# Performance work log

Hardware: AMD Instinct MI355X
Metric: run time of the kernel (lower is better)

Reference implementation:

```python
import jax, jax.numpy as jnp
import numpy as np

D_MODEL = 1024
NUM_HEADS = 16
D_HEAD = 64
D_MLP = 4096
SEQ = 2048
BATCH = 4
NEG_BIG = 1e10


def setup_inputs() -> dict:
    key = jax.random.key(0)
    ks = jax.random.split(key, 10)
    s = 1.0 / np.sqrt(D_MODEL)
    return {
        "x": jax.random.normal(ks[0], (BATCH, SEQ, D_MODEL), dtype=jnp.float32),
        "W_K": jax.random.normal(ks[1], (NUM_HEADS, D_HEAD, D_MODEL), dtype=jnp.float32) * s,
        "W_Q": jax.random.normal(ks[2], (NUM_HEADS, D_HEAD, D_MODEL), dtype=jnp.float32) * s,
        "W_V": jax.random.normal(ks[3], (NUM_HEADS, D_HEAD, D_MODEL), dtype=jnp.float32) * s,
        "W_O": jax.random.normal(ks[4], (D_MODEL, D_HEAD * NUM_HEADS), dtype=jnp.float32) * s,
        "W_in": jax.random.normal(ks[5], (D_MLP, D_MODEL), dtype=jnp.float32) * s,
        "b_in": jnp.zeros((D_MLP,), dtype=jnp.float32),
        "W_out": jax.random.normal(ks[6], (D_MODEL, D_MLP), dtype=jnp.float32) * s,
        "b_out": jnp.zeros((D_MODEL,), dtype=jnp.float32),
    }


def _block(x, W_K, W_Q, W_V, W_O, W_in, b_in, W_out, b_out):
    seq = x.shape[1]
    # Attention
    k = jnp.einsum("ihd,bpd->biph", W_K, x)
    q = jnp.einsum("ihd,bpd->biph", W_Q, x)
    v = jnp.einsum("ihd,bpd->biph", W_V, x)
    scores = jnp.einsum("biph,biqh->biqp", k, q)  # [b, i, q(query), p(key)]
    mask = jnp.tril(jnp.ones((seq, seq), dtype=x.dtype))  # causal: key p <= query q
    scores = scores * mask - NEG_BIG * (1.0 - mask)
    attn = jax.nn.softmax(scores / np.sqrt(D_HEAD), axis=-1)
    z = jnp.einsum("biph,biqp->biqh", v, attn)  # [b, heads, q, d_head]
    z_flat = jnp.transpose(z, (0, 2, 1, 3)).reshape(z.shape[0], seq, -1)  # b q (i h)
    attn_out = jnp.einsum("df,bqf->bqd", W_O, z_flat)
    x = x + attn_out
    # MLP
    h = jnp.einsum("md,bpd->bpm", W_in, x) + b_in
    h = jax.nn.gelu(h, approximate=False)
    mlp_out = jnp.einsum("dm,bpm->bpd", W_out, h) + b_out
    return x + mlp_out


def reference(x, W_K, W_Q, W_V, W_O, W_in, b_in, W_out, b_out):
    return _block(x, W_K, W_Q, W_V, W_O, W_in, b_in, W_out, b_out)
```

## Files before the change

### kernel.cpp

```cpp
#include <hip/hip_runtime.h>
#include <hip/hip_bf16.h>

typedef __bf16 bf16;
typedef __bf16 bf16x8 __attribute__((ext_vector_type(8)));
typedef __bf16 bf16x4 __attribute__((ext_vector_type(4)));
typedef float  f32x4  __attribute__((ext_vector_type(4)));

#define MFMA(a,b,c) __builtin_amdgcn_mfma_f32_16x16x32_bf16(a,b,c,0,0,0)
#define EXP2F(x) __builtin_amdgcn_exp2f(x)

__device__ __forceinline__ void gload16(const void* g, void* l) {
  __builtin_amdgcn_global_load_lds((__attribute__((address_space(1))) void*)(g),
                                   (__attribute__((address_space(3))) void*)(l), 16, 0, 0);
}

__global__ void cast_kernel(const float* __restrict__ in, bf16* __restrict__ out, int n8) {
  int i = blockIdx.x * 256 + threadIdx.x;
  if (i >= n8) return;
  const float4* p = (const float4*)in;
  float4 a = p[2*i], b = p[2*i+1];
  bf16x8 v;
  v[0]=(bf16)a.x; v[1]=(bf16)a.y; v[2]=(bf16)a.z; v[3]=(bf16)a.w;
  v[4]=(bf16)b.x; v[5]=(bf16)b.y; v[6]=(bf16)b.z; v[7]=(bf16)b.w;
  *(bf16x8*)(out + (size_t)8*i) = v;
}

__device__ __forceinline__ float gelu_t(float s) {
  float u = s * (0.7978845608f + 0.0356774081f * s * s);
  return s / (1.0f + EXP2F(-2.885390082f * u));
}

#define LGKM0_FENCE() { asm volatile("s_waitcnt lgkmcnt(0)" ::: "memory"); \
                        __builtin_amdgcn_sched_barrier(0); }

#define LDA_PH(MI2) { _Pragma("unroll") for (int i = 0; i < 4; i++) { \
    af[i][0] = *(const bf16x8*)(lds + ab + ((((MI2)<<2)+i) << 11) + rdswz); \
    af[i][1] = *(const bf16x8*)(lds + ab + ((((MI2)<<2)+i) << 11) + 1024 + rdswz); } }

#define LDB_PH(NI2) { _Pragma("unroll") for (int n = 0; n < 2; n++) { \
    bfr[((NI2)<<1)+n][0] = *(const bf16x8*)(lds + bb + (((((NI2)<<1)+n)) << 11) + rdswz); \
    bfr[((NI2)<<1)+n][1] = *(const bf16x8*)(lds + bb + (((((NI2)<<1)+n)) << 11) + 1024 + rdswz); } }

#define MM_PH(MI2, NI2) { __builtin_amdgcn_s_setprio(1); \
    _Pragma("unroll") for (int i = 0; i < 4; i++) \
      _Pragma("unroll") for (int n = 0; n < 2; n++) { \
        acc[((MI2)<<2)+i][((NI2)<<1)+n] = MFMA(af[i][0], bfr[((NI2)<<1)+n][0], acc[((MI2)<<2)+i][((NI2)<<1)+n]); \
        acc[((MI2)<<2)+i][((NI2)<<1)+n] = MFMA(af[i][1], bfr[((NI2)<<1)+n][1], acc[((MI2)<<2)+i][((NI2)<<1)+n]); } \
    __builtin_amdgcn_s_setprio(0); }

#define GTILE(CUR, S1, S2, VM) { \
    const int ab = ((CUR) << 16) + (wm << 14); \
    const int bb = ((CUR) << 16) + 32768 + (wn << 13); \
    LDA_PH(0); LDB_PH(0); \
    if (S1) STG(sA, (CUR)^1, 0, 1, t + 1); \
    asm volatile("s_waitcnt lgkmcnt(8)" ::: "memory"); \
    __builtin_amdgcn_s_barrier(); LGKM0_FENCE(); \
    MM_PH(0, 0); \
    LDB_PH(1); \
    if (S2) STG(sB, (CUR), 1, 0, t + 2); \
    __builtin_amdgcn_s_barrier(); LGKM0_FENCE(); \
    MM_PH(0, 1); \
    LDA_PH(1); \
    if (S2) STG(sB, (CUR), 1, 1, t + 2); \
    __builtin_amdgcn_s_barrier(); LGKM0_FENCE(); \
    MM_PH(1, 0); \
    if (S2) STG(sA, (CUR), 0, 0, t + 2); \
    MM_PH(1, 1); \
    asm volatile("s_waitcnt vmcnt(" #VM ")" ::: "memory"); \
    __builtin_amdgcn_s_barrier(); \
    __builtin_amdgcn_sched_barrier(0); }

template<int EPI>
__global__ __launch_bounds__(512, 2) void gemm256(
    const bf16* __restrict__ A, const bf16* __restrict__ B,
    float* __restrict__ outf, bf16* __restrict__ outb,
    const float* __restrict__ add, const float* __restrict__ bias,
    bf16* __restrict__ vtb,
    int M, int N, int K, int gx)
{
  __shared__ __attribute__((aligned(128))) char lds[131072];
  const int tid = threadIdx.x;
  const int w = tid >> 6, l = tid & 63, lg = l >> 4, li = l & 15;
  const int wm = w >> 2, wn = w & 3;

  const int nwg = gridDim.x, orig = blockIdx.x;
  const int q = nwg >> 3, r = nwg & 7;
  const int xcd = orig & 7, pos = orig >> 3;
  const int wg = (xcd < r ? xcd*(q+1) : r*(q+1) + (xcd-r)*q) + pos;
  const int m0 = (wg / gx) << 8, n0 = (wg % gx) << 8;

  const int NT = K >> 6;

  const int srow = ((tid >> 7) << 4) + ((tid >> 2) & 15);
  const int scol = (((tid >> 6) & 1) << 5) + (((tid & 3) << 3) ^ (((tid >> 5) & 1) << 4));
  const bf16* sA = A + (size_t)(m0 + srow) * K + scol;
  const bf16* sB = B + (size_t)(n0 + srow) * K + scol;
  char* const myl = lds + (w << 10);

  auto STG = [&](const bf16* s0, int buf, int isB, int h, int tt) {
    const bf16* g = s0 + ((size_t)(h << 7)) * K + ((size_t)tt << 6);
    char* lb = myl + (buf << 16) + (isB << 15) + (h << 14);
    gload16(g, lb);
    gload16(g + ((size_t)K << 6), lb + 8192);
  };

  const int rdswz = (li << 6) + ((lg << 4) ^ ((li & 8) << 2));

  f32x4 acc[8][4] = {};
  bf16x8 af[4][2], bfr[4][2];

  STG(sB, 0, 1, 0, 0); STG(sB, 0, 1, 1, 0); STG(sA, 0, 0, 0, 0); STG(sA, 0, 0, 1, 0);
  asm volatile("s_waitcnt vmcnt(4)" ::: "memory");
  STG(sB, 1, 1, 0, 1); STG(sB, 1, 1, 1, 1); STG(sA, 1, 0, 0, 1);
  asm volatile("s_waitcnt vmcnt(6)" ::: "memory");
  __builtin_amdgcn_s_barrier();
  __builtin_amdgcn_sched_barrier(0);

  int t = 0;
  for (int tt = 0; tt + 3 < NT; tt += 2) {
    t = tt;     GTILE(0, 1, 1, 6);
    t = tt + 1; GTILE(1, 1, 1, 6);
  }
  t = NT - 2; GTILE(0, 1, 0, 0);
  t = NT - 1; GTILE(1, 0, 0, 0);

  if (EPI == 0 && n0 >= 2048) {
    #pragma unroll
    for (int mi = 0; mi < 8; mi++) {
      const int row = m0 + (wm << 7) + (mi << 4) + (lg << 2);
      const int p = row & 2047;
      const size_t bhb = (size_t)((row >> 11) << 4);
      #pragma unroll
      for (int ni = 0; ni < 4; ni++) {
        const int col = n0 + (wn << 6) + (ni << 4) + li;
        const int hh = (col >> 6) & 15, dd = col & 63;
        bf16x4 pk;
        pk[0] = (bf16)acc[mi][ni][0]; pk[1] = (bf16)acc[mi][ni][1];
        pk[2] = (bf16)acc[mi][ni][2]; pk[3] = (bf16)acc[mi][ni][3];
        *(bf16x4*)(vtb + ((bhb + hh) * 64 + dd) * 2048 + p) = pk;
      }
    }
    return;
  }

  #pragma unroll
  for (int mi = 0; mi < 8; mi++) {
    const int row = m0 + (wm << 7) + (mi << 4) + (lg << 2);
    #pragma unroll
    for (int ni = 0; ni < 4; ni++) {
      const int col = n0 + (wn << 6) + (ni << 4) + li;
      #pragma unroll
      for (int r2 = 0; r2 < 4; r2++) {
        const size_t idx = (size_t)(row + r2) * N + col;
        float v = acc[mi][ni][r2];
        if (EPI == 0) {
          outb[idx] = (bf16)v;
        } else if (EPI == 1) {
          float s = v + add[idx];
          outf[idx] = s; outb[idx] = (bf16)s;
        } else if (EPI == 2) {
          outb[idx] = (bf16)gelu_t(v + bias[col]);
        } else {
          outf[idx] = v + bias[col] + add[idx];
        }
      }
    }
  }
}

#define N_LDA2(BMI) { _Pragma("unroll") for (int i = 0; i < 2; i++) { \
    af[i][0] = *(const bf16x8*)(lds + abase + (((BMI)+i) << 11) + rdswz); \
    af[i][1] = *(const bf16x8*)(lds + abase + (((BMI)+i) << 11) + 1024 + rdswz); } }

#define N_LDB2(BNI) { _Pragma("unroll") for (int n = 0; n < 2; n++) { \
    bfr[(BNI)+n][0] = *(const bf16x8*)(lds + bbase + (((BNI)+n) << 11) + rdswz); \
    bfr[(BNI)+n][1] = *(const bf16x8*)(lds + bbase + (((BNI)+n) << 11) + 1024 + rdswz); } }

#define N_MMQ(MB, NB) { __builtin_amdgcn_s_setprio(1); \
    _Pragma("unroll") for (int i = 0; i < 2; i++) \
      _Pragma("unroll") for (int n = 0; n < 2; n++) { \
        acc[((MB)<<1)+i][((NB)<<1)+n] = MFMA(af[i][0], bfr[((NB)<<1)+n][0], acc[((MB)<<1)+i][((NB)<<1)+n]); \
        acc[((MB)<<1)+i][((NB)<<1)+n] = MFMA(af[i][1], bfr[((NB)<<1)+n][1], acc[((MB)<<1)+i][((NB)<<1)+n]); } \
    __builtin_amdgcn_s_setprio(0); }

#define NTILE(CUR, S1, S2, VM) { \
    const int abase = (CUR) * 49152 + ((wm >> 1) << 14) + ((wm & 1) << 13); \
    const int bbase = (CUR) * 49152 + 32768 + (wn << 13); \
    N_LDA2(0); N_LDB2(0); \
    if (S1) STA((CUR)^1, 1, t + 1); \
    __builtin_amdgcn_s_barrier(); LGKM0_FENCE(); \
    N_MMQ(0, 0); \
    N_LDB2(2); \
    if (S2) STB((CUR), 0, t + 2); \
    __builtin_amdgcn_s_barrier(); LGKM0_FENCE(); \
    N_MMQ(0, 1); \
    N_LDA2(2); \
    if (S2) STB((CUR), 1, t + 2); \
    __builtin_amdgcn_s_barrier(); LGKM0_FENCE(); \
    N_MMQ(1, 0); \
    if (S2) STA((CUR), 0, t + 2); \
    N_MMQ(1, 1); \
    asm volatile("s_waitcnt vmcnt(" #VM ")" ::: "memory"); \
    __builtin_amdgcn_s_barrier(); \
    __builtin_amdgcn_sched_barrier(0); }

template<int EPI>
__global__ __launch_bounds__(512, 2) void gemm128n(
    const bf16* __restrict__ A, const bf16* __restrict__ B,
    float* __restrict__ outf, bf16* __restrict__ outb,
    const float* __restrict__ add, const float* __restrict__ bias,
    int M, int N, int K, int gx)
{
  __shared__ __attribute__((aligned(128))) char lds[98304];
  const int tid = threadIdx.x;
  const int w = tid >> 6, l = tid & 63, lg = l >> 4, li = l & 15;
  const int wm = w >> 1, wn = w & 1;

  const int nwg = gridDim.x, orig = blockIdx.x;
  const int q = nwg >> 3, r = nwg & 7;
  const int xcd = orig & 7, pos = orig >> 3;
  const int wg = (xcd < r ? xcd*(q+1) : r*(q+1) + (xcd-r)*q) + pos;
  const int m0 = (wg / gx) << 8, n0 = (wg % gx) << 7;

  const int NT = K >> 6;

  const int srow = ((tid >> 7) << 4) + ((tid >> 2) & 15);
  const int scol = (((tid >> 6) & 1) << 5) + (((tid & 3) << 3) ^ (((tid >> 5) & 1) << 4));
  const bf16* sA = A + (size_t)(m0 + srow) * K + scol;
  const bf16* sB = B + (size_t)(n0 + srow) * K + scol;
  char* const myl = lds + (w << 10);

  auto STA = [&](int buf, int h, int tt) {
    const bf16* g = sA + ((size_t)(h << 7)) * K + ((size_t)tt << 6);
    char* lb = myl + buf * 49152 + (h << 14);
    gload16(g, lb);
    gload16(g + ((size_t)K << 6), lb + 8192);
  };
  auto STB = [&](int buf, int h, int tt) {
    const bf16* g = sB + ((size_t)(h << 6)) * K + ((size_t)tt << 6);
    gload16(g, myl + buf * 49152 + 32768 + (h << 13));
  };

  const int rdswz = (li << 6) + ((lg << 4) ^ ((li & 8) << 2));

  f32x4 acc[4][4] = {};
  bf16x8 af[2][2], bfr[4][2];

  STB(0, 0, 0); STB(0, 1, 0); STA(0, 0, 0); STA(0, 1, 0);
  STB(1, 0, 1); STB(1, 1, 1); STA(1, 0, 1);
  asm volatile("s_waitcnt vmcnt(4)" ::: "memory");
  __builtin_amdgcn_s_barrier();
  __builtin_amdgcn_sched_barrier(0);

  int t = 0;
  for (int tt = 0; tt + 3 < NT; tt += 2) {
    t = tt;     NTILE(0, 1, 1, 4);
    t = tt + 1; NTILE(1, 1, 1, 4);
  }
  t = NT - 2; NTILE(0, 1, 0, 0);
  t = NT - 1; NTILE(1, 0, 0, 0);

  #pragma unroll
  for (int mi = 0; mi < 4; mi++) {
    const int row = m0 + (wm << 6) + (mi << 4) + (lg << 2);
    #pragma unroll
    for (int ni = 0; ni < 4; ni++) {
      const int col = n0 + (wn << 6) + (ni << 4) + li;
      #pragma unroll
      for (int r2 = 0; r2 < 4; r2++) {
        const size_t idx = (size_t)(row + r2) * N + col;
        float v = acc[mi][ni][r2];
        if (EPI == 0) {
          outb[idx] = (bf16)v;
        } else if (EPI == 1) {
          float s = v + add[idx];
          outf[idx] = s; outb[idx] = (bf16)s;
        } else if (EPI == 2) {
          outb[idx] = (bf16)gelu_t(v + bias[col]);
        } else {
          outf[idx] = v + bias[col] + add[idx];
        }
      }
    }
  }
}

__global__ __launch_bounds__(256) void attn_kernel(const bf16* __restrict__ qkv,
                                                   const bf16* __restrict__ vt,
                                                   bf16* __restrict__ z)
{
  __shared__ bf16 Ksh[2][64*64];
  __shared__ bf16 Vsh[2][64*64];
  __shared__ bf16 Pl[4*16*64];

  const int tid = threadIdx.x;
  const int w = tid >> 6, l = tid & 63, lg = l >> 4, li = l & 15;
  const int pr = blockIdx.x & 15, bh = blockIdx.x >> 4;
  const int h = bh & 15, b = bh >> 4;
  const size_t tb = (size_t)b * 2048;

  const int srow = tid >> 3, sc = tid & 7;
  const bf16* Kg = qkv + (tb + srow) * 3072 + 1024 + (h << 6) + ((sc ^ (srow & 7)) << 3);
  const bf16* Vg = vt + ((size_t)bh * 64 + srow) * 2048 + ((sc ^ (srow & 7)) << 3);

  char* pw = (char*)Pl + (w << 11) + li * 128;
  const int psw = (li & 3) << 5;

  for (int hf = 0; hf < 2; ++hf) {
    const int qt = hf ? pr : (31 - pr);
    const int qw = (qt << 6) + (w << 4);

    const bf16* Qp = qkv + (tb + qw + li) * 3072 + (h << 6);
    bf16x8 qa0 = *(const bf16x8*)(Qp + (lg << 3));
    bf16x8 qa1 = *(const bf16x8*)(Qp + 32 + (lg << 3));
    #pragma unroll
    for (int e = 0; e < 8; e++) {
      qa0[e] = (bf16)((float)qa0[e] * 0.1803368801f);
      qa1[e] = (bf16)((float)qa1[e] * 0.1803368801f);
    }

    f32x4 zacc[4] = {};
    float mR = -1e30f, lS = 0.f;
    const int nkt = qt + 1;

    gload16(Kg,                   (bf16*)Ksh[0] + (w << 9));
    gload16(Kg + (size_t)32*3072, (bf16*)Ksh[0] + 2048 + (w << 9));
    gload16(Vg,                   (bf16*)Vsh[0] + (w << 9));
    gload16(Vg + (size_t)32*2048, (bf16*)Vsh[0] + 2048 + (w << 9));
    __syncthreads();

    for (int kt = 0; kt < nkt; ++kt) {
      const int cur = kt & 1;
      const int pb = kt << 6;

      if (kt + 1 < nkt) {
        const int nb = cur ^ 1;
        const size_t ko = (size_t)(pb + 64) * 3072;
        gload16(Kg + ko,                   (bf16*)Ksh[nb] + (w << 9));
        gload16(Kg + ko + (size_t)32*3072, (bf16*)Ksh[nb] + 2048 + (w << 9));
        gload16(Vg + pb + 64,                   (bf16*)Vsh[nb] + (w << 9));
        gload16(Vg + pb + 64 + (size_t)32*2048, (bf16*)Vsh[nb] + 2048 + (w << 9));
      }

      f32x4 s[4];
      __builtin_amdgcn_s_setprio(1);
      #pragma unroll
      for (int sub = 0; sub < 4; ++sub) {
        const char* kr = (const char*)Ksh[cur] + ((sub << 4) + li) * 128;
        const int c0 = (lg ^ (li & 7)) << 4;
        bf16x8 kb0 = *(const bf16x8*)(kr + c0);
        bf16x8 kb1 = *(const bf16x8*)(kr + (c0 ^ 64));
        f32x4 a2 = {};
        a2 = MFMA(kb0, qa0, a2);
        a2 = MFMA(kb1, qa1, a2);
        s[sub] = a2;
      }
      __builtin_amdgcn_s_setprio(0);

      if (pb + 63 > qw) {
        #pragma unroll
        for (int sub = 0; sub < 4; ++sub)
          #pragma unroll
          for (int r = 0; r < 4; ++r)
            if (pb + (sub << 4) + (lg << 2) + r > qw + li) s[sub][r] = -1e30f;
      }

      f32x4 m4;
      #pragma unroll
      for (int r = 0; r < 4; ++r)
        m4[r] = fmaxf(fmaxf(s[0][r], s[1][r]), fmaxf(s[2][r], s[3][r]));
      float mx = fmaxf(fmaxf(m4[0], m4[1]), fmaxf(m4[2], m4[3]));
      mx = fmaxf(mx, __shfl_xor(mx, 16));
      mx = fmaxf(mx, __shfl_xor(mx, 32));

      float mn = mR;
      if (!__all(mx <= mR + 11.5f)) {
        mn = fmaxf(mR, mx);
        float c = EXP2F(mR - mn);
        mR = mn;
        lS *= c;
        float cr0 = __shfl(c, (lg << 2) + 0);
        float cr1 = __shfl(c, (lg << 2) + 1);
        float cr2 = __shfl(c, (lg << 2) + 2);
        float cr3 = __shfl(c, (lg << 2) + 3);
        #pragma unroll
        for (int d = 0; d < 4; ++d) {
          zacc[d][0] *= cr0; zacc[d][1] *= cr1;
          zacc[d][2] *= cr2; zacc[d][3] *= cr3;
        }
      }

      f32x4 p[4];
      #pragma unroll
      for (int sub = 0; sub < 4; ++sub)
        #pragma unroll
        for (int r = 0; r < 4; ++r)
          p[sub][r] = EXP2F(s[sub][r] - mn);
      f32x4 t4 = p[0] + p[1] + p[2] + p[3];
      lS += (t4[0] + t4[1]) + (t4[2] + t4[3]);

      #pragma unroll
      for (int sub = 0; sub < 4; ++sub) {
        bf16x4 pk;
        pk[0] = (bf16)p[sub][0]; pk[1] = (bf16)p[sub][1];
        pk[2] = (bf16)p[sub][2]; pk[3] = (bf16)p[sub][3];
        *(bf16x4*)(pw + (((sub << 5) + (lg << 3)) ^ psw)) = pk;
      }

      __builtin_amdgcn_s_setprio(1);
      #pragma unroll
      for (int kc = 0; kc < 2; ++kc) {
        bf16x8 pa = *(const bf16x8*)(pw + (((kc << 6) + (lg << 4)) ^ psw));
        #pragma unroll
        for (int d = 0; d < 4; ++d) {
          const char* vr = (const char*)Vsh[cur] + ((d << 4) + li) * 128;
          bf16x8 vb = *(const bf16x8*)(vr + ((((kc << 2) + lg) ^ (li & 7)) << 4));
          zacc[d] = MFMA(pa, vb, zacc[d]);
        }
      }
      __builtin_amdgcn_s_setprio(0);

      __syncthreads();
    }

    lS += __shfl_xor(lS, 16);
    lS += __shfl_xor(lS, 32);

    float rls[4];
    #pragma unroll
    for (int r = 0; r < 4; ++r) rls[r] = 1.0f / __shfl(lS, (lg << 2) + r);
    bf16* zp = z + (tb + qw) * 1024 + (h << 6);
    #pragma unroll
    for (int d = 0; d < 4; ++d)
      #pragma unroll
      for (int r = 0; r < 4; ++r)
        zp[(size_t)((lg << 2) + r) * 1024 + (d << 4) + li] = (bf16)(zacc[d][r] * rls[r]);
  }
}

extern "C" void kernel_launch(void* const* d_in, const int* in_sizes, int n_in,
                              void* d_out, int out_size, void* d_ws, size_t ws_size,
                              hipStream_t stream)
{
  const float* x     = (const float*)d_in[0];
  const float* W_K   = (const float*)d_in[1];
  const float* W_Q   = (const float*)d_in[2];
  const float* W_V   = (const float*)d_in[3];
  const float* W_O   = (const float*)d_in[4];
  const float* W_in  = (const float*)d_in[5];
  const float* b_in  = (const float*)d_in[6];
  const float* W_out = (const float*)d_in[7];
  const float* b_out = (const float*)d_in[8];
  float* out = (float*)d_out;

  char* ws = (char*)d_ws;
  bf16*  xb   = (bf16*)ws;  ws += (size_t)8192*1024*2;
  bf16*  wqkv = (bf16*)ws;  ws += (size_t)3072*1024*2;
  bf16*  wo   = (bf16*)ws;  ws += (size_t)1024*1024*2;
  bf16*  win  = (bf16*)ws;  ws += (size_t)4096*1024*2;
  bf16*  wout = (bf16*)ws;  ws += (size_t)1024*4096*2;
  bf16*  qkv  = (bf16*)ws;  ws += (size_t)8192*3072*2;
  bf16*  zb   = (bf16*)ws;  ws += (size_t)8192*1024*2;
  float* x1f  = (float*)ws; ws += (size_t)8192*1024*4;
  bf16*  x1b  = (bf16*)ws;  ws += (size_t)8192*1024*2;
  bf16*  hb   = (bf16*)ws;
  bf16*  vtb  = hb;

  auto cast = [&](const float* src, bf16* dst, size_t n) {
    int n8 = (int)(n / 8);
    cast_kernel<<<dim3((n8 + 255) / 256), dim3(256), 0, stream>>>(src, dst, n8);
  };
  cast(x,     xb,               (size_t)8192*1024);
  cast(W_Q,   wqkv,             (size_t)1024*1024);
  cast(W_K,   wqkv + 1024*1024, (size_t)1024*1024);
  cast(W_V,   wqkv + 2048*1024, (size_t)1024*1024);
  cast(W_O,   wo,               (size_t)1024*1024);
  cast(W_in,  win,              (size_t)4096*1024);
  cast(W_out, wout,             (size_t)1024*4096);

  gemm256<0><<<dim3(384), 512, 0, stream>>>(xb, wqkv, nullptr, qkv, nullptr, nullptr, vtb, 8192, 3072, 1024, 12);
  attn_kernel<<<dim3(1024), 256, 0, stream>>>(qkv, vtb, zb);
  gemm128n<1><<<dim3(256), 512, 0, stream>>>(zb, wo, x1f, x1b, x, nullptr, 8192, 1024, 1024, 8);
  gemm256<2><<<dim3(512), 512, 0, stream>>>(x1b, win, nullptr, hb, nullptr, b_in, nullptr, 8192, 4096, 1024, 16);
  gemm128n<3><<<dim3(256), 512, 0, stream>>>(hb, wout, out, nullptr, x1f, b_out, 8192, 1024, 4096, 8);
}
```

Measured before the change: 335.0 us.

## Merge casts into one launch, use 256x128 tiles for QKV, remap attention blocks per XCD

The seven separate cast launches become one multi-segment cast kernel that picks its source and destination from a prefix-sum table. The QKV projection moves from the 256x256 GEMM (384 blocks) to the 256x128 GEMM (768 blocks), and the V-transpose epilogue moves with it. The attention grid is remapped so that all 16 query blocks of a batch-head land on the same XCD, aiming for better L2 reuse of K/V. These changes target launch overhead, wave quantization on the QKV GEMM and cross-XCD cache misses, at the cost of smaller QKV tiles with less operand reuse.

```diff
diff --git a/kernel.cpp b/kernel.cpp
--- a/kernel.cpp
+++ b/kernel.cpp
@@ -14,15 +14,25 @@
                                    (__attribute__((address_space(3))) void*)(l), 16, 0, 0);
 }
 
-__global__ void cast_kernel(const float* __restrict__ in, bf16* __restrict__ out, int n8) {
+struct CastSegs {
+  const float* src[7];
+  bf16* dst[7];
+  int cum[8];
+};
+
+__global__ void cast_multi(CastSegs s) {
   int i = blockIdx.x * 256 + threadIdx.x;
-  if (i >= n8) return;
-  const float4* p = (const float4*)in;
-  float4 a = p[2*i], b = p[2*i+1];
+  if (i >= s.cum[7]) return;
+  int k = 0;
+  #pragma unroll
+  for (int j = 1; j < 7; ++j) if (i >= s.cum[j]) k = j;
+  int off = i - s.cum[k];
+  const float4* p = (const float4*)s.src[k];
+  float4 a = p[2*off], b = p[2*off+1];
   bf16x8 v;
   v[0]=(bf16)a.x; v[1]=(bf16)a.y; v[2]=(bf16)a.z; v[3]=(bf16)a.w;
   v[4]=(bf16)b.x; v[5]=(bf16)b.y; v[6]=(bf16)b.z; v[7]=(bf16)b.w;
-  *(bf16x8*)(out + (size_t)8*i) = v;
+  *(bf16x8*)(s.dst[k] + (size_t)8*off) = v;
 }
 
 __device__ __forceinline__ float gelu_t(float s) {
@@ -75,7 +85,6 @@
     const bf16* __restrict__ A, const bf16* __restrict__ B,
     float* __restrict__ outf, bf16* __restrict__ outb,
     const float* __restrict__ add, const float* __restrict__ bias,
-    bf16* __restrict__ vtb,
     int M, int N, int K, int gx)
 {
   __shared__ __attribute__((aligned(128))) char lds[131072];
@@ -123,25 +132,6 @@
   }
   t = NT - 2; GTILE(0, 1, 0, 0);
   t = NT - 1; GTILE(1, 0, 0, 0);
-
-  if (EPI == 0 && n0 >= 2048) {
-    #pragma unroll
-    for (int mi = 0; mi < 8; mi++) {
-      const int row = m0 + (wm << 7) + (mi << 4) + (lg << 2);
-      const int p = row & 2047;
-      const size_t bhb = (size_t)((row >> 11) << 4);
-      #pragma unroll
-      for (int ni = 0; ni < 4; ni++) {
-        const int col = n0 + (wn << 6) + (ni << 4) + li;
-        const int hh = (col >> 6) & 15, dd = col & 63;
-        bf16x4 pk;
-        pk[0] = (bf16)acc[mi][ni][0]; pk[1] = (bf16)acc[mi][ni][1];
-        pk[2] = (bf16)acc[mi][ni][2]; pk[3] = (bf16)acc[mi][ni][3];
-        *(bf16x4*)(vtb + ((bhb + hh) * 64 + dd) * 2048 + p) = pk;
-      }
-    }
-    return;
-  }
 
   #pragma unroll
   for (int mi = 0; mi < 8; mi++) {
@@ -209,6 +199,7 @@
     const bf16* __restrict__ A, const bf16* __restrict__ B,
     float* __restrict__ outf, bf16* __restrict__ outb,
     const float* __restrict__ add, const float* __restrict__ bias,
+    bf16* __restrict__ vtb,
     int M, int N, int K, int gx)
 {
   __shared__ __attribute__((aligned(128))) char lds[98304];
@@ -259,6 +250,25 @@
   }
   t = NT - 2; NTILE(0, 1, 0, 0);
   t = NT - 1; NTILE(1, 0, 0, 0);
+
+  if (EPI == 0 && n0 >= 2048) {
+    #pragma unroll
+    for (int mi = 0; mi < 4; mi++) {
+      const int row = m0 + (wm << 6) + (mi << 4) + (lg << 2);
+      const int p = row & 2047;
+      const size_t bhb = (size_t)((row >> 11) << 4);
+      #pragma unroll
+      for (int ni = 0; ni < 4; ni++) {
+        const int col = n0 + (wn << 6) + (ni << 4) + li;
+        const int hh = (col >> 6) & 15, dd = col & 63;
+        bf16x4 pk;
+        pk[0] = (bf16)acc[mi][ni][0]; pk[1] = (bf16)acc[mi][ni][1];
+        pk[2] = (bf16)acc[mi][ni][2]; pk[3] = (bf16)acc[mi][ni][3];
+        *(bf16x4*)(vtb + ((bhb + hh) * 64 + dd) * 2048 + p) = pk;
+      }
+    }
+    return;
+  }
 
   #pragma unroll
   for (int mi = 0; mi < 4; mi++) {
@@ -295,7 +305,10 @@
 
   const int tid = threadIdx.x;
   const int w = tid >> 6, l = tid & 63, lg = l >> 4, li = l & 15;
-  const int pr = blockIdx.x & 15, bh = blockIdx.x >> 4;
+  const int orig = blockIdx.x;
+  const int xcd = orig & 7, sub = orig >> 3;
+  const int bh = (xcd << 3) + (sub >> 4);
+  const int pr = sub & 15;
   const int h = bh & 15, b = bh >> 4;
   const size_t tb = (size_t)b * 2048;
 
@@ -345,24 +358,24 @@
       f32x4 s[4];
       __builtin_amdgcn_s_setprio(1);
       #pragma unroll
-      for (int sub = 0; sub < 4; ++sub) {
-        const char* kr = (const char*)Ksh[cur] + ((sub << 4) + li) * 128;
+      for (int sub2 = 0; sub2 < 4; ++sub2) {
+        const char* kr = (const char*)Ksh[cur] + ((sub2 << 4) + li) * 128;
         const int c0 = (lg ^ (li & 7)) << 4;
         bf16x8 kb0 = *(const bf16x8*)(kr + c0);
         bf16x8 kb1 = *(const bf16x8*)(kr + (c0 ^ 64));
         f32x4 a2 = {};
         a2 = MFMA(kb0, qa0, a2);
         a2 = MFMA(kb1, qa1, a2);
-        s[sub] = a2;
+        s[sub2] = a2;
       }
       __builtin_amdgcn_s_setprio(0);
 
       if (pb + 63 > qw) {
         #pragma unroll
-        for (int sub = 0; sub < 4; ++sub)
+        for (int sub2 = 0; sub2 < 4; ++sub2)
           #pragma unroll
           for (int r = 0; r < 4; ++r)
-            if (pb + (sub << 4) + (lg << 2) + r > qw + li) s[sub][r] = -1e30f;
+            if (pb + (sub2 << 4) + (lg << 2) + r > qw + li) s[sub2][r] = -1e30f;
       }
 
       f32x4 m4;
@@ -392,19 +405,19 @@
 
       f32x4 p[4];
       #pragma unroll
-      for (int sub = 0; sub < 4; ++sub)
+      for (int sub2 = 0; sub2 < 4; ++sub2)
         #pragma unroll
         for (int r = 0; r < 4; ++r)
-          p[sub][r] = EXP2F(s[sub][r] - mn);
+          p[sub2][r] = EXP2F(s[sub2][r] - mn);
       f32x4 t4 = p[0] + p[1] + p[2] + p[3];
       lS += (t4[0] + t4[1]) + (t4[2] + t4[3]);
 
       #pragma unroll
-      for (int sub = 0; sub < 4; ++sub) {
+      for (int sub2 = 0; sub2 < 4; ++sub2) {
         bf16x4 pk;
-        pk[0] = (bf16)p[sub][0]; pk[1] = (bf16)p[sub][1];
-        pk[2] = (bf16)p[sub][2]; pk[3] = (bf16)p[sub][3];
-        *(bf16x4*)(pw + (((sub << 5) + (lg << 3)) ^ psw)) = pk;
+        pk[0] = (bf16)p[sub2][0]; pk[1] = (bf16)p[sub2][1];
+        pk[2] = (bf16)p[sub2][2]; pk[3] = (bf16)p[sub2][3];
+        *(bf16x4*)(pw + (((sub2 << 5) + (lg << 3)) ^ psw)) = pk;
       }
 
       __builtin_amdgcn_s_setprio(1);
@@ -466,21 +479,18 @@
   bf16*  hb   = (bf16*)ws;
   bf16*  vtb  = hb;
 
-  auto cast = [&](const float* src, bf16* dst, size_t n) {
-    int n8 = (int)(n / 8);
-    cast_kernel<<<dim3((n8 + 255) / 256), dim3(256), 0, stream>>>(src, dst, n8);
-  };
-  cast(x,     xb,               (size_t)8192*1024);
-  cast(W_Q,   wqkv,             (size_t)1024*1024);
-  cast(W_K,   wqkv + 1024*1024, (size_t)1024*1024);
-  cast(W_V,   wqkv + 2048*1024, (size_t)1024*1024);
-  cast(W_O,   wo,               (size_t)1024*1024);
-  cast(W_in,  win,              (size_t)4096*1024);
-  cast(W_out, wout,             (size_t)1024*4096);
-
-  gemm256<0><<<dim3(384), 512, 0, stream>>>(xb, wqkv, nullptr, qkv, nullptr, nullptr, vtb, 8192, 3072, 1024, 12);
+  CastSegs cs;
+  const float* srcs[7] = { x, W_Q, W_K, W_V, W_O, W_in, W_out };
+  bf16* dsts[7] = { xb, wqkv, wqkv + 1024*1024, wqkv + 2048*1024, wo, win, wout };
+  int n8s[7] = { 1048576, 131072, 131072, 131072, 131072, 524288, 524288 };
+  int cum = 0;
+  for (int i = 0; i < 7; ++i) { cs.src[i] = srcs[i]; cs.dst[i] = dsts[i]; cs.cum[i] = cum; cum += n8s[i]; }
+  cs.cum[7] = cum;
+  cast_multi<<<dim3((cum + 255) / 256), dim3(256), 0, stream>>>(cs);
+
+  gemm128n<0><<<dim3(768), 512, 0, stream>>>(xb, wqkv, nullptr, qkv, nullptr, nullptr, vtb, 8192, 3072, 1024, 24);
   attn_kernel<<<dim3(1024), 256, 0, stream>>>(qkv, vtb, zb);
-  gemm128n<1><<<dim3(256), 512, 0, stream>>>(zb, wo, x1f, x1b, x, nullptr, 8192, 1024, 1024, 8);
-  gemm256<2><<<dim3(512), 512, 0, stream>>>(x1b, win, nullptr, hb, nullptr, b_in, nullptr, 8192, 4096, 1024, 16);
-  gemm128n<3><<<dim3(256), 512, 0, stream>>>(hb, wout, out, nullptr, x1f, b_out, 8192, 1024, 4096, 8);
-}
+  gemm128n<1><<<dim3(256), 512, 0, stream>>>(zb, wo, x1f, x1b, x, nullptr, nullptr, 8192, 1024, 1024, 8);
+  gemm256<2><<<dim3(512), 512, 0, stream>>>(x1b, win, nullptr, hb, nullptr, b_in, 8192, 4096, 1024, 16);
+  gemm128n<3><<<dim3(256), 512, 0, stream>>>(hb, wout, out, nullptr, x1f, b_out, nullptr, 8192, 1024, 4096, 8);
+}
```

After: 310.4 us. 1.08x faster.
